# Performance work log

Hardware: AMD Instinct MI355X
Metric: run time of the kernel (lower is better)

Reference implementation:

```python
import jax, jax.numpy as jnp
import numpy as np

N = 100000   # nodes
E = 1600000  # edges
D = 64       # in_features == out_features (residual requires equality)
BN_EPS = 1e-5


def setup_inputs() -> dict:
    key = jax.random.key(0)
    ks = jax.random.split(key, 12)
    s = 1.0 / np.sqrt(D)
    inp = {
        "x": jax.random.normal(ks[0], (N, D), dtype=jnp.float32),
        "edge_index": jax.random.randint(ks[1], (2, E), 0, N, dtype=jnp.int64),
        # ResGatedGraphConv params: key/query/value/skip linears
        "Wk": jax.random.uniform(ks[2], (D, D), jnp.float32, -s, s),
        "bk": jax.random.uniform(ks[3], (D,), jnp.float32, -s, s),
        "Wq": jax.random.uniform(ks[4], (D, D), jnp.float32, -s, s),
        "bq": jax.random.uniform(ks[5], (D,), jnp.float32, -s, s),
        "Wv": jax.random.uniform(ks[6], (D, D), jnp.float32, -s, s),
        "bv": jax.random.uniform(ks[7], (D,), jnp.float32, -s, s),
        "Ws": jax.random.uniform(ks[8], (D, D), jnp.float32, -s, s),
        "bs": jax.random.uniform(ks[9], (D,), jnp.float32, -s, s),
        # BatchNorm1d affine params
        "gamma": jnp.ones((D,), jnp.float32),
        "beta": jnp.zeros((D,), jnp.float32),
    }
    return inp


def reference(x, edge_index, Wk, bk, Wq, bq, Wv, bv, Ws, bs, gamma, beta):
    # PyG ResGatedGraphConv:
    #   out_i = W_s x_i + b_s + sum_{(j->i)} sigmoid(k_i + q_j) * v_j
    # where k = lin_key(x), q = lin_query(x), v = lin_value(x).
    src = edge_index[0]  # source nodes j
    dst = edge_index[1]  # target nodes i

    k = x @ Wk.T + bk  # [N, D]
    q = x @ Wq.T + bq  # [N, D]
    v = x @ Wv.T + bv  # [N, D]

    gate = jax.nn.sigmoid(k[dst] + q[src])        # [E, D]
    msg = gate * v[src]                            # [E, D]
    agg = jax.ops.segment_sum(msg, dst, num_segments=x.shape[0])  # [N, D]

    h = agg + x @ Ws.T + bs

    # BatchNorm1d (training mode: batch statistics, biased variance)
    mean = jnp.mean(h, axis=0)
    var = jnp.var(h, axis=0)
    h = (h - mean) * jax.lax.rsqrt(var + BN_EPS) * gamma + beta

    h = jax.nn.relu(h)
    h = h + x  # residual
    # dropout: identity in eval / deterministic reference
    return h
```

## Files before the change

kernel.cpp:

```cpp
#include <hip/hip_runtime.h>
#include <hip/hip_bf16.h>
#include <math.h>

#define N_NODES 100000
#define N_EDGES 1600000
#define D_FEAT  64
#define BN_EPS  1e-5f

#define NBUCKET_PAD 256
#define BUCKET_SHIFT 9
#define NBLK_E  196
#define EPB     8192
#define HIST_TOTAL (NBUCKET_PAD * NBLK_E)
#define NCHUNK_H 98
#define DCAP    14336

typedef __attribute__((ext_vector_type(8))) short bf16x8;
typedef __attribute__((ext_vector_type(4))) float f32x4;

static __device__ __forceinline__ short f2bf(float f) {
    __hip_bfloat16 h = __float2bfloat16(f);
    return __builtin_bit_cast(short, h);
}


__global__ __launch_bounds__(256) void gemm4_mfma_kernel(
    const float* __restrict__ x,
    const float* __restrict__ Wk, const float* __restrict__ bk,
    const float* __restrict__ Wq, const float* __restrict__ bq,
    const float* __restrict__ Wv, const float* __restrict__ bv,
    const float* __restrict__ Ws, const float* __restrict__ bs,
    unsigned short* __restrict__ qvp,
    unsigned short* __restrict__ kp,
    float* __restrict__ h0)
{
    __shared__ short xs[64 * 64];

    const int lane = threadIdx.x & 63;
    const int wave = threadIdx.x >> 6;
    const int r0 = blockIdx.x * 64;

    const float* W; const float* b;
    if      (wave == 0) { W = Wk; b = bk; }
    else if (wave == 1) { W = Wq; b = bq; }
    else if (wave == 2) { W = Wv; b = bv; }
    else                { W = Ws; b = bs; }

    const int bcol = lane & 15;
    const int bk0  = (lane >> 4) * 8;
    bf16x8 bfrag[4][2];
    #pragma unroll
    for (int nt = 0; nt < 4; ++nt) {
        #pragma unroll
        for (int ks = 0; ks < 2; ++ks) {
            const float* wp = W + (nt * 16 + bcol) * 64 + ks * 32 + bk0;
            const float4 w0 = *reinterpret_cast<const float4*>(wp);
            const float4 w1 = *reinterpret_cast<const float4*>(wp + 4);
            bf16x8 f;
            f[0] = f2bf(w0.x); f[1] = f2bf(w0.y); f[2] = f2bf(w0.z); f[3] = f2bf(w0.w);
            f[4] = f2bf(w1.x); f[5] = f2bf(w1.y); f[6] = f2bf(w1.z); f[7] = f2bf(w1.w);
            bfrag[nt][ks] = f;
        }
    }
    float biasv[4];
    #pragma unroll
    for (int nt = 0; nt < 4; ++nt) biasv[nt] = b[nt * 16 + bcol];

    {
        const int row = threadIdx.x >> 2;
        const int qd  = threadIdx.x & 3;
        const int grow = r0 + row;
        float4 t0, t1, t2, t3;
        if (grow < N_NODES) {
            const float* xp = x + (size_t)grow * 64 + qd * 16;
            t0 = reinterpret_cast<const float4*>(xp)[0];
            t1 = reinterpret_cast<const float4*>(xp)[1];
            t2 = reinterpret_cast<const float4*>(xp)[2];
            t3 = reinterpret_cast<const float4*>(xp)[3];
        } else {
            t0 = t1 = t2 = t3 = make_float4(0.f, 0.f, 0.f, 0.f);
        }
        bf16x8 u0, u1;
        u0[0] = f2bf(t0.x); u0[1] = f2bf(t0.y); u0[2] = f2bf(t0.z); u0[3] = f2bf(t0.w);
        u0[4] = f2bf(t1.x); u0[5] = f2bf(t1.y); u0[6] = f2bf(t1.z); u0[7] = f2bf(t1.w);
        u1[0] = f2bf(t2.x); u1[1] = f2bf(t2.y); u1[2] = f2bf(t2.z); u1[3] = f2bf(t2.w);
        u1[4] = f2bf(t3.x); u1[5] = f2bf(t3.y); u1[6] = f2bf(t3.z); u1[7] = f2bf(t3.w);
        const int sw = row & 7;
        *reinterpret_cast<bf16x8*>(xs + row * 64 + (((qd * 2)     ^ sw) * 8)) = u0;
        *reinterpret_cast<bf16x8*>(xs + row * 64 + (((qd * 2 + 1) ^ sw) * 8)) = u1;
    }
    __syncthreads();

    f32x4 acc[4][4];
    #pragma unroll
    for (int mt = 0; mt < 4; ++mt)
        #pragma unroll
        for (int nt = 0; nt < 4; ++nt)
            acc[mt][nt] = (f32x4){biasv[nt], biasv[nt], biasv[nt], biasv[nt]};

    const int arow = lane & 15;
    const int ak   = lane >> 4;
    #pragma unroll
    for (int mt = 0; mt < 4; ++mt) {
        const int row = mt * 16 + arow;
        const int sw = row & 7;
        const bf16x8 a0 = *reinterpret_cast<const bf16x8*>(xs + row * 64 + ((ak       ^ sw) * 8));
        const bf16x8 a1 = *reinterpret_cast<const bf16x8*>(xs + row * 64 + (((4 + ak) ^ sw) * 8));
        #pragma unroll
        for (int nt = 0; nt < 4; ++nt) {
            acc[mt][nt] = __builtin_amdgcn_mfma_f32_16x16x32_bf16(
                a0, bfrag[nt][0], acc[mt][nt], 0, 0, 0);
            acc[mt][nt] = __builtin_amdgcn_mfma_f32_16x16x32_bf16(
                a1, bfrag[nt][1], acc[mt][nt], 0, 0, 0);
        }
    }

    const int crow0 = (lane >> 4) * 4;
    const int ccol  = lane & 15;
    #pragma unroll
    for (int mt = 0; mt < 4; ++mt) {
        #pragma unroll
        for (int nt = 0; nt < 4; ++nt) {
            #pragma unroll
            for (int r = 0; r < 4; ++r) {
                const int grow = r0 + mt * 16 + crow0 + r;
                if (grow < N_NODES) {
                    const int col = nt * 16 + ccol;
                    const float val = acc[mt][nt][r];
                    const size_t idx = (size_t)grow * 64 + col;
                    if      (wave == 0) kp[idx] = (unsigned short)f2bf(val);
                    else if (wave == 1) qvp[idx * 2]     = (unsigned short)f2bf(val);
                    else if (wave == 2) qvp[idx * 2 + 1] = (unsigned short)f2bf(val);
                    else                h0[idx] = val;
                }
            }
        }
    }
}

__global__ __launch_bounds__(256) void bucket_count_kernel(
    const int* __restrict__ ei, int* __restrict__ blockhist)
{
    __shared__ int h[NBUCKET_PAD];
    h[threadIdx.x] = 0;
    __syncthreads();
    const int base = blockIdx.x * EPB;
    for (int i = threadIdx.x; i < EPB; i += 256) {
        const int e = base + i;
        if (e < N_EDGES) atomicAdd(&h[ei[N_EDGES + e] >> BUCKET_SHIFT], 1);
    }
    __syncthreads();
    blockhist[threadIdx.x * NBLK_E + blockIdx.x] = h[threadIdx.x];
}

__global__ __launch_bounds__(256) void scan1_kernel(
    int* __restrict__ buf, int* __restrict__ chunk_sums, int total)
{
    __shared__ int sh[256];
    const int t = threadIdx.x;
    const int base = blockIdx.x * 512;
    const int i0 = base + 2 * t, i1 = base + 2 * t + 1;
    const int a = (i0 < total) ? buf[i0] : 0;
    const int b = (i1 < total) ? buf[i1] : 0;
    const int s = a + b;
    sh[t] = s;
    __syncthreads();
    for (int off = 1; off < 256; off <<= 1) {
        const int val = (t >= off) ? sh[t - off] : 0;
        __syncthreads();
        sh[t] += val;
        __syncthreads();
    }
    const int excl = sh[t] - s;
    if (i0 < total) buf[i0] = excl;
    if (i1 < total) buf[i1] = excl + a;
    if (t == 255) chunk_sums[blockIdx.x] = sh[255];
}

__global__ __launch_bounds__(256) void scan2_kernel(
    const int* __restrict__ chunk_sums, int* __restrict__ chunk_off, int nchunk)
{
    __shared__ int sh[256];
    const int t = threadIdx.x;
    const int v = (t < nchunk) ? chunk_sums[t] : 0;
    sh[t] = v;
    __syncthreads();
    for (int off = 1; off < 256; off <<= 1) {
        const int val = (t >= off) ? sh[t - off] : 0;
        __syncthreads();
        sh[t] += val;
        __syncthreads();
    }
    if (t < nchunk) chunk_off[t] = sh[t] - v;
}

__global__ __launch_bounds__(256) void scan3_kernel(
    int* __restrict__ buf, const int* __restrict__ chunk_off, int total)
{
    const int off = chunk_off[blockIdx.x];
    const int base = blockIdx.x * 512;
    #pragma unroll
    for (int k = 0; k < 2; ++k) {
        const int i = base + k * 256 + threadIdx.x;
        if (i < total) buf[i] += off;
    }
}

__global__ __launch_bounds__(256) void bucket_scatter_kernel(
    const int* __restrict__ ei, const int* __restrict__ blockhist,
    unsigned int* __restrict__ tmp)
{
    __shared__ int cur[NBUCKET_PAD];
    cur[threadIdx.x] = blockhist[threadIdx.x * NBLK_E + blockIdx.x];
    __syncthreads();
    const int base = blockIdx.x * EPB;
    for (int i = threadIdx.x; i < EPB; i += 256) {
        const int e = base + i;
        if (e < N_EDGES) {
            const int s = ei[e];
            const int d = ei[N_EDGES + e];
            const int pos = atomicAdd(&cur[d >> BUCKET_SHIFT], 1);
            tmp[pos] = ((unsigned int)s << BUCKET_SHIFT) | (unsigned int)(d & 511);
        }
    }
}

__global__ __launch_bounds__(512) void bucket_sort_kernel(
    const int* __restrict__ blockhist,
    unsigned int* __restrict__ tmp,
    int* __restrict__ row_start)
{
    __shared__ unsigned int stage[DCAP];
    __shared__ int hist[512];
    __shared__ int cursor[512];
    const int b = blockIdx.x;
    const int t = threadIdx.x;
    const int bstart = blockhist[b * NBLK_E];
    const int bend   = blockhist[(b + 1) * NBLK_E];
    int sz = bend - bstart;
    if (sz > DCAP) sz = DCAP;
    for (int i = t; i < sz; i += 512) stage[i] = tmp[bstart + i];
    hist[t] = 0;
    __syncthreads();
    for (int i = t; i < sz; i += 512) atomicAdd(&hist[stage[i] & 511], 1);
    __syncthreads();
    const int myv = hist[t];
    for (int off = 1; off < 512; off <<= 1) {
        const int u = (t >= off) ? hist[t - off] : 0;
        __syncthreads();
        hist[t] += u;
        __syncthreads();
    }
    const int excl = hist[t] - myv;
    const int node = b * 512 + t;
    if (node <= N_NODES) row_start[node] = bstart + excl;
    cursor[t] = excl;
    __syncthreads();
    for (int i = t; i < sz; i += 512) {
        const unsigned int pk = stage[i];
        const int pos = atomicAdd(&cursor[(int)(pk & 511)], 1);
        tmp[bstart + pos] = pk >> BUCKET_SHIFT;
    }
}

#define EDGE_F(u, kfj, accj) {                                        \
    const float qf_ = __uint_as_float((u) << 16);                     \
    const float vf_ = __uint_as_float((u) & 0xffff0000u);             \
    const float e_  = __expf(-((kfj) + qf_));                         \
    (accj) = fmaf(__builtin_amdgcn_rcpf(1.0f + e_), vf_, (accj)); }

__global__ __launch_bounds__(256, 4) void gather_kernel(
    const unsigned int* __restrict__ qv,
    const unsigned short* __restrict__ kp,
    const int* __restrict__ row_start,
    const int* __restrict__ sorted_src,
    float* __restrict__ h0, float* __restrict__ stats)
{
    const int lane = threadIdx.x & 63;
    const int sub  = lane >> 4;
    const int l    = lane & 15;
    const int wave = threadIdx.x >> 6;

    float4 lsum = make_float4(0.f, 0.f, 0.f, 0.f);
    float4 lsq  = make_float4(0.f, 0.f, 0.f, 0.f);

    const int quad0  = blockIdx.x * 4 + wave;
    const int qstride = gridDim.x * 4;
    const int nquads = N_NODES / 4;

    for (int quad = quad0; quad < nquads; quad += qstride) {
        const int n = quad * 4 + sub;
        const int base = row_start[n];
        const int end  = row_start[n + 1];
        const int deg  = end - base;

        int m1 = max(deg, __shfl_xor(deg, 16));
        const int maxdeg = max(m1, __shfl_xor(m1, 32));

        const ushort4 kr = *reinterpret_cast<const ushort4*>(kp + (size_t)n * 64 + 4 * l);
        float4 kf;
        kf.x = __uint_as_float((unsigned int)kr.x << 16);
        kf.y = __uint_as_float((unsigned int)kr.y << 16);
        kf.z = __uint_as_float((unsigned int)kr.z << 16);
        kf.w = __uint_as_float((unsigned int)kr.w << 16);
        float4 acc = *reinterpret_cast<const float4*>(h0 + (size_t)n * 64 + 4 * l);

        const int safe_last = max(min(end - 1, N_EDGES - 1), 0);

        for (int t = 0; t < maxdeg; t += 4) {
            const int i0 = min(base + t + 0, safe_last);
            const int i1 = min(base + t + 1, safe_last);
            const int i2 = min(base + t + 2, safe_last);
            const int i3 = min(base + t + 3, safe_last);
            const int s0 = sorted_src[i0];
            const int s1 = sorted_src[i1];
            const int s2 = sorted_src[i2];
            const int s3 = sorted_src[i3];
            uint4 U0 = *reinterpret_cast<const uint4*>(qv + (size_t)s0 * 64 + 4 * l);
            uint4 U1 = *reinterpret_cast<const uint4*>(qv + (size_t)s1 * 64 + 4 * l);
            uint4 U2 = *reinterpret_cast<const uint4*>(qv + (size_t)s2 * 64 + 4 * l);
            uint4 U3 = *reinterpret_cast<const uint4*>(qv + (size_t)s3 * 64 + 4 * l);
            const bool v0 = (t + 0) < deg, v1 = (t + 1) < deg,
                       v2 = (t + 2) < deg, v3 = (t + 3) < deg;
            U0.x = v0 ? U0.x : 0u; U0.y = v0 ? U0.y : 0u; U0.z = v0 ? U0.z : 0u; U0.w = v0 ? U0.w : 0u;
            U1.x = v1 ? U1.x : 0u; U1.y = v1 ? U1.y : 0u; U1.z = v1 ? U1.z : 0u; U1.w = v1 ? U1.w : 0u;
            U2.x = v2 ? U2.x : 0u; U2.y = v2 ? U2.y : 0u; U2.z = v2 ? U2.z : 0u; U2.w = v2 ? U2.w : 0u;
            U3.x = v3 ? U3.x : 0u; U3.y = v3 ? U3.y : 0u; U3.z = v3 ? U3.z : 0u; U3.w = v3 ? U3.w : 0u;

            EDGE_F(U0.x, kf.x, acc.x) EDGE_F(U0.y, kf.y, acc.y)
            EDGE_F(U0.z, kf.z, acc.z) EDGE_F(U0.w, kf.w, acc.w)
            EDGE_F(U1.x, kf.x, acc.x) EDGE_F(U1.y, kf.y, acc.y)
            EDGE_F(U1.z, kf.z, acc.z) EDGE_F(U1.w, kf.w, acc.w)
            EDGE_F(U2.x, kf.x, acc.x) EDGE_F(U2.y, kf.y, acc.y)
            EDGE_F(U2.z, kf.z, acc.z) EDGE_F(U2.w, kf.w, acc.w)
            EDGE_F(U3.x, kf.x, acc.x) EDGE_F(U3.y, kf.y, acc.y)
            EDGE_F(U3.z, kf.z, acc.z) EDGE_F(U3.w, kf.w, acc.w)
        }

        *reinterpret_cast<float4*>(h0 + (size_t)n * 64 + 4 * l) = acc;
        lsum.x += acc.x; lsum.y += acc.y; lsum.z += acc.z; lsum.w += acc.w;
        lsq.x += acc.x * acc.x; lsq.y += acc.y * acc.y;
        lsq.z += acc.z * acc.z; lsq.w += acc.w * acc.w;
    }

    __shared__ float bsum[64];
    __shared__ float bsq[64];
    if (threadIdx.x < 64) { bsum[threadIdx.x] = 0.f; bsq[threadIdx.x] = 0.f; }
    __syncthreads();
    atomicAdd(&bsum[4 * l + 0], lsum.x); atomicAdd(&bsq[4 * l + 0], lsq.x);
    atomicAdd(&bsum[4 * l + 1], lsum.y); atomicAdd(&bsq[4 * l + 1], lsq.y);
    atomicAdd(&bsum[4 * l + 2], lsum.z); atomicAdd(&bsq[4 * l + 2], lsq.z);
    atomicAdd(&bsum[4 * l + 3], lsum.w); atomicAdd(&bsq[4 * l + 3], lsq.w);
    __syncthreads();
    if (threadIdx.x < 64) {
        atomicAdd(&stats[threadIdx.x], bsum[threadIdx.x]);
        atomicAdd(&stats[64 + threadIdx.x], bsq[threadIdx.x]);
    }
}

__global__ __launch_bounds__(256) void final_kernel(
    float* __restrict__ h0, const float* __restrict__ x,
    const float* __restrict__ stats,
    const float* __restrict__ gamma, const float* __restrict__ beta)
{
    const float invN = 1.0f / (float)N_NODES;
    const long long total = (long long)N_NODES * D_FEAT;
    for (long long idx = (long long)blockIdx.x * 256 + threadIdx.x;
         idx < total; idx += (long long)gridDim.x * 256) {
        const int i = (int)(idx & 63);
        const float mean = stats[i] * invN;
        const float var  = stats[64 + i] * invN - mean * mean;
        const float rstd = rsqrtf(var + BN_EPS);
        float y = (h0[idx] - mean) * rstd * gamma[i] + beta[i];
        y = fmaxf(y, 0.0f) + x[idx];
        h0[idx] = y;
    }
}

extern "C" void kernel_launch(void* const* d_in, const int* in_sizes, int n_in,
                              void* d_out, int out_size, void* d_ws, size_t ws_size,
                              hipStream_t stream)
{
    const float* x     = (const float*)d_in[0];
    const int*   ei    = (const int*)d_in[1];
    const float* Wk    = (const float*)d_in[2];
    const float* bk    = (const float*)d_in[3];
    const float* Wq    = (const float*)d_in[4];
    const float* bq    = (const float*)d_in[5];
    const float* Wv    = (const float*)d_in[6];
    const float* bv    = (const float*)d_in[7];
    const float* Ws    = (const float*)d_in[8];
    const float* bs    = (const float*)d_in[9];
    const float* gamma = (const float*)d_in[10];
    const float* beta  = (const float*)d_in[11];

    char* w = (char*)d_ws;
    unsigned int*   qv   = (unsigned int*)w;
    unsigned short* kpl  = (unsigned short*)(w + 25600000);
    float* stats      = (float*)(w + 38400000);
    int*   blockhist  = (int*)  (w + 38400512);
    int*   chunk_sums = (int*)  (w + 38601216);
    int*   chunk_off  = (int*)  (w + 38601608);
    int*   row_start  = (int*)  (w + 38602000);
    unsigned int* tmp = (unsigned int*)(w + 39002004);

    float* h0 = (float*)d_out;

    hipMemsetAsync(stats, 0, 128 * sizeof(float), stream);

    gemm4_mfma_kernel<<<(N_NODES + 63) / 64, 256, 0, stream>>>(
        x, Wk, bk, Wq, bq, Wv, bv, Ws, bs, (unsigned short*)qv, kpl, h0);

    bucket_count_kernel<<<NBLK_E, 256, 0, stream>>>(ei, blockhist);
    scan1_kernel<<<NCHUNK_H, 256, 0, stream>>>(blockhist, chunk_sums, HIST_TOTAL);
    scan2_kernel<<<1, 256, 0, stream>>>(chunk_sums, chunk_off, NCHUNK_H);
    scan3_kernel<<<NCHUNK_H, 256, 0, stream>>>(blockhist, chunk_off, HIST_TOTAL);
    bucket_scatter_kernel<<<NBLK_E, 256, 0, stream>>>(ei, blockhist, tmp);
    bucket_sort_kernel<<<196, 512, 0, stream>>>(blockhist, tmp, row_start);

    gather_kernel<<<2084, 256, 0, stream>>>(qv, kpl, row_start, (const int*)tmp, h0, stats);

    final_kernel<<<2048, 256, 0, stream>>>(h0, x, stats, gamma, beta);
}
```

Before: 219.0 us.

## Fuse bucket count into GEMM launch, stage bf16 outputs in LDS, vectorize final

The bucket-count pass now runs as extra blocks of the GEMM kernel, so one launch does both jobs and the two can overlap. The GEMM's k/q/v outputs are staged as bf16 in shared-memory tiles and then written with 16-byte vector stores instead of scattered 2-byte stores. The final BN/ReLU/residual kernel now uses float4 loads and stores and precomputes the per-column scale. This raises shared-memory use per GEMM block and mixes two kinds of block in one grid.

```diff
diff --git a/kernel.cpp b/kernel.cpp
--- a/kernel.cpp
+++ b/kernel.cpp
@@ -14,6 +14,7 @@
 #define HIST_TOTAL (NBUCKET_PAD * NBLK_E)
 #define NCHUNK_H 98
 #define DCAP    14336
+#define GEMM_BLOCKS 1563
 
 typedef __attribute__((ext_vector_type(8))) short bf16x8;
 typedef __attribute__((ext_vector_type(4))) float f32x4;
@@ -24,17 +25,36 @@
 }
 
 
-__global__ __launch_bounds__(256) void gemm4_mfma_kernel(
+__global__ __launch_bounds__(256) void gemm4_count_kernel(
     const float* __restrict__ x,
     const float* __restrict__ Wk, const float* __restrict__ bk,
     const float* __restrict__ Wq, const float* __restrict__ bq,
     const float* __restrict__ Wv, const float* __restrict__ bv,
     const float* __restrict__ Ws, const float* __restrict__ bs,
-    unsigned short* __restrict__ qvp,
+    unsigned int* __restrict__ qv,
     unsigned short* __restrict__ kp,
-    float* __restrict__ h0)
+    float* __restrict__ h0,
+    const int* __restrict__ ei, int* __restrict__ blockhist)
 {
     __shared__ short xs[64 * 64];
+    __shared__ unsigned short kt[64][68];
+    __shared__ unsigned short qt[64][68];
+    __shared__ unsigned short vt[64][68];
+    __shared__ int hcnt[NBUCKET_PAD];
+
+    if (blockIdx.x >= GEMM_BLOCKS) {
+        const int cb = blockIdx.x - GEMM_BLOCKS;
+        hcnt[threadIdx.x] = 0;
+        __syncthreads();
+        const int base = cb * EPB;
+        for (int i = threadIdx.x; i < EPB; i += 256) {
+            const int e = base + i;
+            if (e < N_EDGES) atomicAdd(&hcnt[ei[N_EDGES + e] >> BUCKET_SHIFT], 1);
+        }
+        __syncthreads();
+        blockhist[threadIdx.x * NBLK_E + cb] = hcnt[threadIdx.x];
+        return;
+    }
 
     const int lane = threadIdx.x & 63;
     const int wave = threadIdx.x >> 6;
@@ -117,40 +137,57 @@
 
     const int crow0 = (lane >> 4) * 4;
     const int ccol  = lane & 15;
-    #pragma unroll
-    for (int mt = 0; mt < 4; ++mt) {
+    if (wave < 3) {
+        unsigned short (*tile)[68] = (wave == 0) ? kt : (wave == 1) ? qt : vt;
         #pragma unroll
-        for (int nt = 0; nt < 4; ++nt) {
+        for (int mt = 0; mt < 4; ++mt)
             #pragma unroll
-            for (int r = 0; r < 4; ++r) {
-                const int grow = r0 + mt * 16 + crow0 + r;
-                if (grow < N_NODES) {
-                    const int col = nt * 16 + ccol;
-                    const float val = acc[mt][nt][r];
-                    const size_t idx = (size_t)grow * 64 + col;
-                    if      (wave == 0) kp[idx] = (unsigned short)f2bf(val);
-                    else if (wave == 1) qvp[idx * 2]     = (unsigned short)f2bf(val);
-                    else if (wave == 2) qvp[idx * 2 + 1] = (unsigned short)f2bf(val);
-                    else                h0[idx] = val;
+            for (int nt = 0; nt < 4; ++nt)
+                #pragma unroll
+                for (int r = 0; r < 4; ++r)
+                    tile[mt * 16 + crow0 + r][nt * 16 + ccol] =
+                        (unsigned short)f2bf(acc[mt][nt][r]);
+    } else {
+        #pragma unroll
+        for (int mt = 0; mt < 4; ++mt)
+            #pragma unroll
+            for (int nt = 0; nt < 4; ++nt)
+                #pragma unroll
+                for (int r = 0; r < 4; ++r) {
+                    const int grow = r0 + mt * 16 + crow0 + r;
+                    if (grow < N_NODES)
+                        h0[(size_t)grow * 64 + nt * 16 + ccol] = acc[mt][nt][r];
                 }
-            }
-        }
-    }
-}
-
-__global__ __launch_bounds__(256) void bucket_count_kernel(
-    const int* __restrict__ ei, int* __restrict__ blockhist)
-{
-    __shared__ int h[NBUCKET_PAD];
-    h[threadIdx.x] = 0;
-    __syncthreads();
-    const int base = blockIdx.x * EPB;
-    for (int i = threadIdx.x; i < EPB; i += 256) {
-        const int e = base + i;
-        if (e < N_EDGES) atomicAdd(&h[ei[N_EDGES + e] >> BUCKET_SHIFT], 1);
-    }
-    __syncthreads();
-    blockhist[threadIdx.x * NBLK_E + blockIdx.x] = h[threadIdx.x];
+    }
+    __syncthreads();
+
+    {
+        const int row = threadIdx.x >> 2;
+        const int seg = threadIdx.x & 3;
+        const int grow = r0 + row;
+        if (grow < N_NODES) {
+            const int c0 = seg * 16;
+            unsigned int qd[16];
+            #pragma unroll
+            for (int i = 0; i < 16; ++i)
+                qd[i] = (unsigned int)qt[row][c0 + i] |
+                        ((unsigned int)vt[row][c0 + i] << 16);
+            uint4* qdst = reinterpret_cast<uint4*>(qv + (size_t)grow * 64 + c0);
+            qdst[0] = make_uint4(qd[0],  qd[1],  qd[2],  qd[3]);
+            qdst[1] = make_uint4(qd[4],  qd[5],  qd[6],  qd[7]);
+            qdst[2] = make_uint4(qd[8],  qd[9],  qd[10], qd[11]);
+            qdst[3] = make_uint4(qd[12], qd[13], qd[14], qd[15]);
+
+            unsigned int kd[8];
+            #pragma unroll
+            for (int i = 0; i < 8; ++i)
+                kd[i] = (unsigned int)kt[row][c0 + 2 * i] |
+                        ((unsigned int)kt[row][c0 + 2 * i + 1] << 16);
+            uint4* kdst = reinterpret_cast<uint4*>(kp + (size_t)grow * 64 + c0);
+            kdst[0] = make_uint4(kd[0], kd[1], kd[2], kd[3]);
+            kdst[1] = make_uint4(kd[4], kd[5], kd[6], kd[7]);
+        }
+    }
 }
 
 __global__ __launch_bounds__(256) void scan1_kernel(
@@ -363,17 +400,39 @@
     const float* __restrict__ stats,
     const float* __restrict__ gamma, const float* __restrict__ beta)
 {
+    const int lane = threadIdx.x & 63;
+    const int sub  = lane >> 4;
+    const int l    = lane & 15;
+    const int wave = threadIdx.x >> 6;
+
     const float invN = 1.0f / (float)N_NODES;
-    const long long total = (long long)N_NODES * D_FEAT;
-    for (long long idx = (long long)blockIdx.x * 256 + threadIdx.x;
-         idx < total; idx += (long long)gridDim.x * 256) {
-        const int i = (int)(idx & 63);
-        const float mean = stats[i] * invN;
-        const float var  = stats[64 + i] * invN - mean * mean;
-        const float rstd = rsqrtf(var + BN_EPS);
-        float y = (h0[idx] - mean) * rstd * gamma[i] + beta[i];
-        y = fmaxf(y, 0.0f) + x[idx];
-        h0[idx] = y;
+    const float4 s1 = *reinterpret_cast<const float4*>(stats + 4 * l);
+    const float4 s2 = *reinterpret_cast<const float4*>(stats + 64 + 4 * l);
+    const float4 g  = *reinterpret_cast<const float4*>(gamma + 4 * l);
+    const float4 bt = *reinterpret_cast<const float4*>(beta + 4 * l);
+    float4 mean, a;
+    mean.x = s1.x * invN; mean.y = s1.y * invN;
+    mean.z = s1.z * invN; mean.w = s1.w * invN;
+    a.x = rsqrtf(s2.x * invN - mean.x * mean.x + BN_EPS) * g.x;
+    a.y = rsqrtf(s2.y * invN - mean.y * mean.y + BN_EPS) * g.y;
+    a.z = rsqrtf(s2.z * invN - mean.z * mean.z + BN_EPS) * g.z;
+    a.w = rsqrtf(s2.w * invN - mean.w * mean.w + BN_EPS) * g.w;
+
+    const int quad0  = blockIdx.x * 4 + wave;
+    const int qstride = gridDim.x * 4;
+    const int nquads = N_NODES / 4;
+
+    for (int quad = quad0; quad < nquads; quad += qstride) {
+        const int n = quad * 4 + sub;
+        const size_t off = (size_t)n * 64 + 4 * l;
+        const float4 h  = *reinterpret_cast<const float4*>(h0 + off);
+        const float4 xx = *reinterpret_cast<const float4*>(x + off);
+        float4 y;
+        y.x = fmaxf((h.x - mean.x) * a.x + bt.x, 0.f) + xx.x;
+        y.y = fmaxf((h.y - mean.y) * a.y + bt.y, 0.f) + xx.y;
+        y.z = fmaxf((h.z - mean.z) * a.z + bt.z, 0.f) + xx.z;
+        y.w = fmaxf((h.w - mean.w) * a.w + bt.w, 0.f) + xx.w;
+        *reinterpret_cast<float4*>(h0 + off) = y;
     }
 }
 
@@ -408,10 +467,9 @@
 
     hipMemsetAsync(stats, 0, 128 * sizeof(float), stream);
 
-    gemm4_mfma_kernel<<<(N_NODES + 63) / 64, 256, 0, stream>>>(
-        x, Wk, bk, Wq, bq, Wv, bv, Ws, bs, (unsigned short*)qv, kpl, h0);
-
-    bucket_count_kernel<<<NBLK_E, 256, 0, stream>>>(ei, blockhist);
+    gemm4_count_kernel<<<GEMM_BLOCKS + NBLK_E, 256, 0, stream>>>(
+        x, Wk, bk, Wq, bq, Wv, bv, Ws, bs, qv, kpl, h0, ei, blockhist);
+
     scan1_kernel<<<NCHUNK_H, 256, 0, stream>>>(blockhist, chunk_sums, HIST_TOTAL);
     scan2_kernel<<<1, 256, 0, stream>>>(chunk_sums, chunk_off, NCHUNK_H);
     scan3_kernel<<<NCHUNK_H, 256, 0, stream>>>(blockhist, chunk_off, HIST_TOTAL);
@@ -420,5 +478,5 @@
 
     gather_kernel<<<2084, 256, 0, stream>>>(qv, kpl, row_start, (const int*)tmp, h0, stats);
 
-    final_kernel<<<2048, 256, 0, stream>>>(h0, x, stats, gamma, beta);
-}
+    final_kernel<<<2084, 256, 0, stream>>>(h0, x, stats, gamma, beta);
+}
```

New measurement: 200.4 us. 1.09x faster.
